# Optimization experiments

Measured on AMD Instinct MI355X. Metric: run time of the kernel, lower is better.

The kernel has to match this reference:

```python
import jax, jax.numpy as jnp
import numpy as np

N, E, D, H, G, C = 50000, 600000, 128, 128, 512, 1000
HP = H // 5  # attention-MLP bottleneck (hidden_dim // 5)


def setup_inputs() -> dict:
    key = jax.random.key(0)
    ks = jax.random.split(key, 18)
    cfg_nodes = jax.random.normal(ks[0], (N, D), jnp.float32)
    cfg_relations = jax.random.randint(ks[1], (2, E), 0, N, dtype=jnp.int32)
    pos = jnp.sort(jax.random.randint(ks[2], (G + 1,), 0, N, dtype=jnp.int32))
    node_pos = pos.at[0].set(0).at[-1].set(N)

    def lin(k, fi, fo):
        return jax.random.normal(k, (fi, fo), jnp.float32) / np.sqrt(fi)

    return dict(
        cfg_nodes=cfg_nodes, cfg_relations=cfg_relations, node_pos=node_pos,
        # GATConv layer 1 (in=D, out=H, heads=1)
        W_g1=lin(ks[3], D, H),
        att_src1=jax.random.normal(ks[4], (H,), jnp.float32) / np.sqrt(H),
        att_dst1=jax.random.normal(ks[5], (H,), jnp.float32) / np.sqrt(H),
        b_g1=jnp.zeros((H,), jnp.float32),
        # GATConv layer 2 (in=H, out=H, heads=1, concat=False)
        W_g2=lin(ks[6], H, H),
        att_src2=jax.random.normal(ks[7], (H,), jnp.float32) / np.sqrt(H),
        att_dst2=jax.random.normal(ks[8], (H,), jnp.float32) / np.sqrt(H),
        b_g2=jnp.zeros((H,), jnp.float32),
        # GraphLocalAttention projection MLP
        Wp1=lin(ks[9], H, HP), bp1=jnp.zeros((HP,), jnp.float32),
        Wp2=jax.random.normal(ks[10], (HP,), jnp.float32) / np.sqrt(HP),
        bp2=jnp.zeros((), jnp.float32),
        # final classifier
        Wl=lin(ks[11], H, C), bl=jnp.zeros((C,), jnp.float32),
    )


def _gat_conv(x, src, dst, W, a_src, a_dst, b, n_nodes):
    # PyG GATConv (heads=1): h = xW; e_ij = LeakyReLU(a_s.h_j + a_d.h_i);
    # alpha = softmax over incoming edges of each target; out_i = sum alpha*h_j + b
    h = x @ W                                    # [N, F]
    as_ = h @ a_src                              # [N]
    ad_ = h @ a_dst                              # [N]
    e = jax.nn.leaky_relu(as_[src] + ad_[dst], 0.2)   # [E]
    m = jax.ops.segment_max(e, dst, num_segments=n_nodes)
    ex = jnp.exp(e - m[dst])
    s = jax.ops.segment_sum(ex, dst, num_segments=n_nodes)
    alpha = ex / s[dst]
    out = jax.ops.segment_sum(alpha[:, None] * h[src], dst, num_segments=n_nodes)
    return out + b


def reference(cfg_nodes, cfg_relations, node_pos,
              W_g1, att_src1, att_dst1, b_g1,
              W_g2, att_src2, att_dst2, b_g2,
              Wp1, bp1, Wp2, bp2, Wl, bl):
    n = cfg_nodes.shape[0]
    # add self-loops (PyG GATConv default)
    loops = jnp.arange(n, dtype=cfg_relations.dtype)
    src = jnp.concatenate([cfg_relations[0], loops])
    dst = jnp.concatenate([cfg_relations[1], loops])
    # dropout layers are identity in eval mode
    x = _gat_conv(cfg_nodes, src, dst, W_g1, att_src1, att_dst1, b_g1, n)
    x = jax.nn.elu(x)
    x = _gat_conv(x, src, dst, W_g2, att_src2, att_dst2, b_g2, n)
    # ragged segment attention pooling (attn_by_batch, fully vectorized)
    energy = jax.nn.relu(x @ Wp1 + bp1) @ Wp2 + bp2          # [N]
    seg = jnp.clip(jnp.searchsorted(node_pos, jnp.arange(n), side='right') - 1, 0, G - 1)
    m = jax.ops.segment_max(energy, seg, num_segments=G)
    ex = jnp.exp(energy - m[seg])
    s = jax.ops.segment_sum(ex, seg, num_segments=G)
    w = ex / s[seg]                                           # per-segment softmax
    pooled = jax.ops.segment_sum(w[:, None] * x, seg, num_segments=G)  # [G, H]
    return pooled @ Wl + bl                                   # [G, C]
```

## Files before the change

### kernel.cpp

```cpp
#include <hip/hip_runtime.h>
#include <hip/hip_bf16.h>
#include <math.h>

#define WAVE 64
#define GR 32

typedef __attribute__((ext_vector_type(8))) _Float16 half8;
typedef __attribute__((ext_vector_type(4))) float f32x4;
typedef __attribute__((ext_vector_type(4))) _Float16 half4;

__global__ void count_pack(const int* __restrict__ dst, int* __restrict__ deg, int E, int nbC,
                           const float* __restrict__ W1, const float* __restrict__ W2,
                           _Float16* __restrict__ W1h, _Float16* __restrict__ W2h,
                           const float* __restrict__ Wp1, int HP,
                           _Float16* __restrict__ Ph) {
    int b = blockIdx.x;
    if (b < nbC) {
        int e = (b * 256 + threadIdx.x) * 2;
        if (e + 1 < E) {
            int2 d = *(const int2*)(dst + e);
            atomicAdd(&deg[d.x], 1);
            atomicAdd(&deg[d.y], 1);
        } else if (e < E) {
            atomicAdd(&deg[dst[e]], 1);
        }
    } else if (b < nbC + 128) {
        int pb = b - nbC;
        const float* W = (pb >= 64) ? W2 : W1;
        _Float16* Hf = (pb >= 64) ? W2h : W1h;
        int idx = (pb & 63) * 256 + threadIdx.x;
        int j = idx & 7;
        int lane = (idx >> 3) & 63;
        int kc = (idx >> 9) & 3;
        int nt = idx >> 11;
        int k = kc * 32 + (lane >> 4) * 8 + j;
        int ncol = nt * 16 + (lane & 15);
        Hf[idx] = (_Float16)W[k * 128 + ncol];
    } else {
        int idx = (b - nbC - 128) * 256 + threadIdx.x;
        int j = idx & 7;
        int lane = (idx >> 3) & 63;
        int kc = (idx >> 9) & 3;
        int nt = idx >> 11;
        int k = kc * 32 + (lane >> 4) * 8 + j;
        int ncol = nt * 16 + (lane & 15);
        float x = (ncol < HP) ? Wp1[k * HP + ncol] : 0.f;
        Ph[idx] = (_Float16)x;
    }
}

__global__ void pack_wl(const float* __restrict__ Wl, int C, _Float16* __restrict__ Wlh) {
    int idx = blockIdx.x * 256 + threadIdx.x;
    int j = idx & 7;
    int lane = (idx >> 3) & 63;
    int kc = (idx >> 9) & 3;
    int nt = idx >> 11;
    int k = kc * 32 + (lane >> 4) * 8 + j;
    int ncol = nt * 16 + (lane & 15);
    float x = (ncol < C) ? Wl[(size_t)k * C + ncol] : 0.f;
    Wlh[idx] = (_Float16)x;
}

__global__ void scan_block(const int* __restrict__ in, int* __restrict__ part,
                           int* __restrict__ bsums, int n) {
    __shared__ int tmp[256];
    int tid = threadIdx.x;
    int i = blockIdx.x * 256 + tid;
    int v = (i < n) ? in[i] : 0;
    tmp[tid] = v;
    __syncthreads();
    for (int o = 1; o < 256; o <<= 1) {
        int t = (tid >= o) ? tmp[tid - o] : 0;
        __syncthreads();
        tmp[tid] += t;
        __syncthreads();
    }
    if (i < n) part[i] = tmp[tid] - v;
    if (tid == 255) bsums[blockIdx.x] = tmp[255];
}

__global__ void scan_finish(const int* __restrict__ part, const int* __restrict__ bsums,
                            int* __restrict__ offs, int* __restrict__ cursor,
                            int n, int Etot) {
    __shared__ int acc[256];
    int b = blockIdx.x, tid = threadIdx.x;
    int s = 0;
    for (int i = tid; i < b; i += 256) s += bsums[i];
    acc[tid] = s;
    __syncthreads();
    for (int o = 128; o > 0; o >>= 1) {
        if (tid < o) acc[tid] += acc[tid + o];
        __syncthreads();
    }
    int prefix = acc[0];
    int i = b * 256 + tid;
    if (i < n) {
        int v = part[i] + prefix;
        offs[i] = v;
        cursor[i] = v;
    }
    if (b == 0 && tid == 0) offs[n] = Etot;
}

__global__ void scatter_edges(const int* __restrict__ src, const int* __restrict__ dst,
                              int* __restrict__ cursor, int* __restrict__ csr_src, int E) {
    int e0 = (blockIdx.x * 256 + threadIdx.x) * 8;
    if (e0 + 7 < E) {
        int4 d0 = *(const int4*)(dst + e0);
        int4 d1 = *(const int4*)(dst + e0 + 4);
        int4 s0 = *(const int4*)(src + e0);
        int4 s1 = *(const int4*)(src + e0 + 4);
        int p0 = atomicAdd(&cursor[d0.x], 1);
        int p1 = atomicAdd(&cursor[d0.y], 1);
        int p2 = atomicAdd(&cursor[d0.z], 1);
        int p3 = atomicAdd(&cursor[d0.w], 1);
        int p4 = atomicAdd(&cursor[d1.x], 1);
        int p5 = atomicAdd(&cursor[d1.y], 1);
        int p6 = atomicAdd(&cursor[d1.z], 1);
        int p7 = atomicAdd(&cursor[d1.w], 1);
        csr_src[p0] = s0.x;
        csr_src[p1] = s0.y;
        csr_src[p2] = s0.z;
        csr_src[p3] = s0.w;
        csr_src[p4] = s1.x;
        csr_src[p5] = s1.y;
        csr_src[p6] = s1.z;
        csr_src[p7] = s1.w;
    } else {
        for (int e = e0; e < E; ++e) {
            int p = atomicAdd(&cursor[dst[e]], 1);
            csr_src[p] = src[e];
        }
    }
}

__global__ __launch_bounds__(256) void gemm_mfma(const float* __restrict__ X,
                                                 const _Float16* __restrict__ Bh,
                                                 const float* __restrict__ a_s,
                                                 const float* __restrict__ a_d,
                                                 _Float16* __restrict__ Hout,
                                                 float* __restrict__ as_,
                                                 float* __restrict__ ad_, int n) {
    __shared__ char lds[GR * 136 * 4];
    _Float16* Xh = (_Float16*)lds;
    float* Hs = (float*)lds;

    int tid = threadIdx.x;
    int base = blockIdx.x * GR;
    const float4* X4 = (const float4*)X;

#pragma unroll
    for (int i = 0; i < 4; ++i) {
        int idx = i * 256 + tid;
        int row = idx >> 5, c4 = idx & 31;
        int rs = base + row; if (rs >= n) rs = n - 1;
        float4 v = X4[(size_t)rs * 32 + c4];
        half4 hv = {(_Float16)v.x, (_Float16)v.y, (_Float16)v.z, (_Float16)v.w};
        *(half4*)(Xh + row * 136 + c4 * 4) = hv;
    }
    __syncthreads();

    int wid = tid >> 6, lane = tid & 63;
    int quad = lane >> 4, l16 = lane & 15;
    int rowA = (wid & 1) * 16 + l16;
    int ntb = (wid >> 1) * 4;

    f32x4 acc[4];
#pragma unroll
    for (int t = 0; t < 4; ++t) acc[t] = (f32x4){0.f, 0.f, 0.f, 0.f};

    for (int kc = 0; kc < 4; ++kc) {
        half8 Ah = *(const half8*)(Xh + rowA * 136 + kc * 32 + quad * 8);
#pragma unroll
        for (int nt = 0; nt < 4; ++nt) {
            half8 Bv = *(const half8*)(Bh + (((size_t)((ntb + nt) * 4 + kc)) * 64 + lane) * 8);
            acc[nt] = __builtin_amdgcn_mfma_f32_16x16x32_f16(Ah, Bv, acc[nt], 0, 0, 0);
        }
    }
    __syncthreads();

    int rowD0 = (wid & 1) * 16 + quad * 4;
#pragma unroll
    for (int nt = 0; nt < 4; ++nt)
#pragma unroll
        for (int r = 0; r < 4; ++r)
            Hs[(rowD0 + r) * 136 + (ntb + nt) * 16 + l16] = acc[nt][r];
    __syncthreads();

    const float4* Hs4 = (const float4*)Hs;
    half4* H4 = (half4*)Hout;
#pragma unroll
    for (int i = 0; i < 4; ++i) {
        int idx = i * 256 + tid;
        int row = idx >> 5, c4 = idx & 31;
        int grow = base + row;
        if (grow < n) {
            float4 v = Hs4[row * 34 + c4];
            half4 hv = {(_Float16)v.x, (_Float16)v.y, (_Float16)v.z, (_Float16)v.w};
            H4[(size_t)grow * 32 + c4] = hv;
        }
    }

    int drow = tid >> 3, q = tid & 7;
    const float4* as4 = (const float4*)a_s;
    const float4* ad4 = (const float4*)a_d;
    float s = 0.f, d = 0.f;
#pragma unroll
    for (int j = 0; j < 4; ++j) {
        float4 v = Hs4[drow * 34 + q * 4 + j];
        float4 a = as4[q * 4 + j];
        float4 b = ad4[q * 4 + j];
        s += v.x * a.x + v.y * a.y + v.z * a.z + v.w * a.w;
        d += v.x * b.x + v.y * b.y + v.z * b.z + v.w * b.w;
    }
    s += __shfl_xor(s, 1, WAVE); s += __shfl_xor(s, 2, WAVE); s += __shfl_xor(s, 4, WAVE);
    d += __shfl_xor(d, 1, WAVE); d += __shfl_xor(d, 2, WAVE); d += __shfl_xor(d, 4, WAVE);
    if (q == 0 && base + drow < n) {
        as_[base + drow] = s;
        ad_[base + drow] = d;
    }
}

__global__ __launch_bounds__(256) void gemm_mfma_h(const _Float16* __restrict__ X,
                                                   const _Float16* __restrict__ Bh,
                                                   const float* __restrict__ a_s,
                                                   const float* __restrict__ a_d,
                                                   _Float16* __restrict__ Hout,
                                                   float* __restrict__ as_,
                                                   float* __restrict__ ad_, int n) {
    __shared__ char lds[GR * 136 * 4];
    _Float16* Xh = (_Float16*)lds;
    float* Hs = (float*)lds;

    int tid = threadIdx.x;
    int base = blockIdx.x * GR;
    const half8* X8 = (const half8*)X;

#pragma unroll
    for (int i = 0; i < 2; ++i) {
        int idx = i * 256 + tid;
        int row = idx >> 4, c8 = idx & 15;
        int rs = base + row; if (rs >= n) rs = n - 1;
        *(half8*)(Xh + row * 136 + c8 * 8) = X8[(size_t)rs * 16 + c8];
    }
    __syncthreads();

    int wid = tid >> 6, lane = tid & 63;
    int quad = lane >> 4, l16 = lane & 15;
    int rowA = (wid & 1) * 16 + l16;
    int ntb = (wid >> 1) * 4;

    f32x4 acc[4];
#pragma unroll
    for (int t = 0; t < 4; ++t) acc[t] = (f32x4){0.f, 0.f, 0.f, 0.f};

    for (int kc = 0; kc < 4; ++kc) {
        half8 Ah = *(const half8*)(Xh + rowA * 136 + kc * 32 + quad * 8);
#pragma unroll
        for (int nt = 0; nt < 4; ++nt) {
            half8 Bv = *(const half8*)(Bh + (((size_t)((ntb + nt) * 4 + kc)) * 64 + lane) * 8);
            acc[nt] = __builtin_amdgcn_mfma_f32_16x16x32_f16(Ah, Bv, acc[nt], 0, 0, 0);
        }
    }
    __syncthreads();

    int rowD0 = (wid & 1) * 16 + quad * 4;
#pragma unroll
    for (int nt = 0; nt < 4; ++nt)
#pragma unroll
        for (int r = 0; r < 4; ++r)
            Hs[(rowD0 + r) * 136 + (ntb + nt) * 16 + l16] = acc[nt][r];
    __syncthreads();

    const float4* Hs4 = (const float4*)Hs;
    half4* H4 = (half4*)Hout;
#pragma unroll
    for (int i = 0; i < 4; ++i) {
        int idx = i * 256 + tid;
        int row = idx >> 5, c4 = idx & 31;
        int grow = base + row;
        if (grow < n) {
            float4 v = Hs4[row * 34 + c4];
            half4 hv = {(_Float16)v.x, (_Float16)v.y, (_Float16)v.z, (_Float16)v.w};
            H4[(size_t)grow * 32 + c4] = hv;
        }
    }

    int drow = tid >> 3, q = tid & 7;
    const float4* as4 = (const float4*)a_s;
    const float4* ad4 = (const float4*)a_d;
    float s = 0.f, d = 0.f;
#pragma unroll
    for (int j = 0; j < 4; ++j) {
        float4 v = Hs4[drow * 34 + q * 4 + j];
        float4 a = as4[q * 4 + j];
        float4 b = ad4[q * 4 + j];
        s += v.x * a.x + v.y * a.y + v.z * a.z + v.w * a.w;
        d += v.x * b.x + v.y * b.y + v.z * b.z + v.w * b.w;
    }
    s += __shfl_xor(s, 1, WAVE); s += __shfl_xor(s, 2, WAVE); s += __shfl_xor(s, 4, WAVE);
    d += __shfl_xor(d, 1, WAVE); d += __shfl_xor(d, 2, WAVE); d += __shfl_xor(d, 4, WAVE);
    if (q == 0 && base + drow < n) {
        as_[base + drow] = s;
        ad_[base + drow] = d;
    }
}

__device__ __forceinline__ float leaky02(float x) { return x > 0.f ? x : 0.2f * x; }

__global__ __launch_bounds__(256) void edge_weights(const int* __restrict__ csr_src,
                                                    const float* __restrict__ as_,
                                                    int2* __restrict__ sw, int E) {
    int i = (blockIdx.x * 256 + threadIdx.x) * 4;
    if (i + 3 < E) {
        int4 s = *(const int4*)(csr_src + i);
        float ax = as_[s.x];
        float ay = as_[s.y];
        float az = as_[s.z];
        float aw = as_[s.w];
        int4 lo = make_int4(s.x, __float_as_int(ax), s.y, __float_as_int(ay));
        int4 hi = make_int4(s.z, __float_as_int(az), s.w, __float_as_int(aw));
        *(int4*)(sw + i) = lo;
        *(int4*)(sw + i + 2) = hi;
    } else {
        for (; i < E; ++i) {
            int s = csr_src[i];
            sw[i] = make_int2(s, __float_as_int(as_[s]));
        }
    }
}

__global__ __launch_bounds__(256) void gat_aggregate(const _Float16* __restrict__ h,
                                                     const int2* __restrict__ sw,
                                                     const float* __restrict__ as_,
                                                     const float* __restrict__ ad_,
                                                     const int* __restrict__ offs,
                                                     const float* __restrict__ bias,
                                                     _Float16* __restrict__ out, int n, int act) {
    int node = blockIdx.x * 4 + (threadIdx.x >> 6);
    int lane = threadIdx.x & 63;
    if (node >= n) return;
    int beg = offs[node], end = offs[node + 1];
    int q4 = lane >> 4, l = lane & 15;
    const half8* h8 = (const half8*)h;

    float adn = ad_[node];
    float w_self = __expf(leaky02(as_[node] + adn));
    float facc[8], facc2[8];
    {
        half8 v = h8[(size_t)node * 16 + l];
        float ws = (q4 == 0) ? w_self : 0.f;
#pragma unroll
        for (int i = 0; i < 8; ++i) { facc[i] = ws * (float)v[i]; facc2[i] = 0.f; }
    }
    float sacc = (lane == 0) ? w_self : 0.f;
    for (int j = beg; j < end; j += 8) {
        int j0 = j + q4;
        int j1 = j + 4 + q4;
        bool vA = j0 < end;
        bool vB = j1 < end;
        int jA = vA ? j0 : (end - 1);
        int jB = vB ? j1 : (end - 1);
        int2 eA = sw[jA];
        int2 eB = sw[jB];
        int sA = vA ? eA.x : node;
        int sB = vB ? eB.x : node;
        half8 a = h8[(size_t)sA * 16 + l];
        half8 b = h8[(size_t)sB * 16 + l];
        float wA = vA ? __expf(leaky02(__int_as_float(eA.y) + adn)) : 0.f;
        float wB = vB ? __expf(leaky02(__int_as_float(eB.y) + adn)) : 0.f;
#pragma unroll
        for (int i = 0; i < 8; ++i) {
            facc[i]  = fmaf(wA, (float)a[i], facc[i]);
            facc2[i] = fmaf(wB, (float)b[i], facc2[i]);
        }
        sacc += (l == 0) ? (wA + wB) : 0.f;
    }
#pragma unroll
    for (int i = 0; i < 8; ++i) {
        facc[i] += facc2[i];
        facc[i] += __shfl_xor(facc[i], 16, WAVE);
        facc[i] += __shfl_xor(facc[i], 32, WAVE);
    }
    sacc += __shfl_xor(sacc, 16, WAVE);
    sacc += __shfl_xor(sacc, 32, WAVE);
    float inv_s = 1.f / __shfl(sacc, 0, WAVE);
    if (q4 == 0) {
        const float4* b4 = (const float4*)bias;
        float4 b0 = b4[l * 2], b1 = b4[l * 2 + 1];
        float o[8];
        o[0] = fmaf(facc[0], inv_s, b0.x);
        o[1] = fmaf(facc[1], inv_s, b0.y);
        o[2] = fmaf(facc[2], inv_s, b0.z);
        o[3] = fmaf(facc[3], inv_s, b0.w);
        o[4] = fmaf(facc[4], inv_s, b1.x);
        o[5] = fmaf(facc[5], inv_s, b1.y);
        o[6] = fmaf(facc[6], inv_s, b1.z);
        o[7] = fmaf(facc[7], inv_s, b1.w);
        if (act == 1) {
#pragma unroll
            for (int i = 0; i < 8; ++i) o[i] = o[i] > 0.f ? o[i] : expm1f(o[i]);
        }
        half8 hv;
#pragma unroll
        for (int i = 0; i < 8; ++i) hv[i] = (_Float16)o[i];
        ((half8*)(out + (size_t)node * 128))[l] = hv;
    }
}

#define GR2 64
__global__ __launch_bounds__(256) void energy_mfma(const _Float16* __restrict__ X,
                                                   const _Float16* __restrict__ Ph,
                                                   const float* __restrict__ bp1,
                                                   const float* __restrict__ Wp2,
                                                   const float* __restrict__ bp2,
                                                   float* __restrict__ energy, int n, int HP) {
    __shared__ _Float16 Xh[GR2 * 136];
    int tid = threadIdx.x;
    int base = blockIdx.x * GR2;
    const half8* X8 = (const half8*)X;
#pragma unroll
    for (int i = 0; i < 4; ++i) {
        int idx = i * 256 + tid;
        int row = idx >> 4, c8 = idx & 15;
        int rs = base + row; if (rs >= n) rs = n - 1;
        *(half8*)(Xh + row * 136 + c8 * 8) = X8[(size_t)rs * 16 + c8];
    }
    __syncthreads();

    int wid = tid >> 6, lane = tid & 63;
    int quad = lane >> 4, l16 = lane & 15;
    int rowA = wid * 16 + l16;

    f32x4 acc0 = (f32x4){0.f, 0.f, 0.f, 0.f};
    f32x4 acc1 = (f32x4){0.f, 0.f, 0.f, 0.f};
    for (int kc = 0; kc < 4; ++kc) {
        half8 Ah = *(const half8*)(Xh + rowA * 136 + kc * 32 + quad * 8);
        half8 B0 = *(const half8*)(Ph + (((size_t)kc) * 64 + lane) * 8);
        half8 B1 = *(const half8*)(Ph + (((size_t)(4 + kc)) * 64 + lane) * 8);
        acc0 = __builtin_amdgcn_mfma_f32_16x16x32_f16(Ah, B0, acc0, 0, 0, 0);
        acc1 = __builtin_amdgcn_mfma_f32_16x16x32_f16(Ah, B1, acc1, 0, 0, 0);
    }

    float b0 = bp1[l16];
    float w0 = Wp2[l16];
    int c1 = 16 + l16;
    int c1c = c1 < HP ? c1 : HP - 1;
    float b1 = bp1[c1c];
    float w1 = (c1 < HP) ? Wp2[c1c] : 0.f;
    float bp2v = bp2[0];
#pragma unroll
    for (int r = 0; r < 4; ++r) {
        float h0 = acc0[r] + b0;
        h0 = h0 > 0.f ? h0 : 0.f;
        float h1 = acc1[r] + b1;
        h1 = h1 > 0.f ? h1 : 0.f;
        float v = h0 * w0 + h1 * w1;
        v += __shfl_xor(v, 1, WAVE);
        v += __shfl_xor(v, 2, WAVE);
        v += __shfl_xor(v, 4, WAVE);
        v += __shfl_xor(v, 8, WAVE);
        int row = base + wid * 16 + quad * 4 + r;
        if (l16 == 0 && row < n) energy[row] = v + bp2v;
    }
}

__global__ __launch_bounds__(256) void seg_pool(const _Float16* __restrict__ X,
                                                const float* __restrict__ energy,
                                                const int* __restrict__ node_pos,
                                                float* __restrict__ pooled) {
    int g = blockIdx.x >> 1;
    int bn = blockIdx.x & 1;
    int beg = node_pos[g], end = node_pos[g + 1];
    int tid = threadIdx.x;
    int wid = tid >> 6, lane = tid & 63;
    __shared__ float swr[8];
    __shared__ float4 red[256];

    float m = -INFINITY;
    for (int i = beg + tid; i < end; i += 256) m = fmaxf(m, energy[i]);
#pragma unroll
    for (int o = 1; o < 64; o <<= 1) m = fmaxf(m, __shfl_xor(m, o, WAVE));
    if (lane == 0) swr[wid] = m;
    __syncthreads();
    m = fmaxf(fmaxf(swr[0], swr[1]), fmaxf(swr[2], swr[3]));

    float s = 0.f;
    for (int i = beg + tid; i < end; i += 256) s += __expf(energy[i] - m);
#pragma unroll
    for (int o = 1; o < 64; o <<= 1) s += __shfl_xor(s, o, WAVE);
    if (lane == 0) swr[4 + wid] = s;
    __syncthreads();
    s = swr[4] + swr[5] + swr[6] + swr[7];
    float inv = (end > beg && s > 0.f) ? 1.f / s : 0.f;

    int cq = tid & 15;
    int rg = tid >> 4;
    const half4* X4 = (const half4*)X;
    float4 acc = make_float4(0.f, 0.f, 0.f, 0.f);
#pragma unroll 2
    for (int i = beg + rg; i < end; i += 16) {
        float w = __expf(energy[i] - m) * inv;
        half4 v = X4[(size_t)i * 32 + bn * 16 + cq];
        acc.x = fmaf(w, (float)v.x, acc.x);
        acc.y = fmaf(w, (float)v.y, acc.y);
        acc.z = fmaf(w, (float)v.z, acc.z);
        acc.w = fmaf(w, (float)v.w, acc.w);
    }
    red[tid] = acc;
#pragma unroll
    for (int o = 8; o >= 1; o >>= 1) {
        __syncthreads();
        if (rg < o) {
            float4 t = red[tid + o * 16];
            acc.x += t.x; acc.y += t.y; acc.z += t.z; acc.w += t.w;
            red[tid] = acc;
        }
    }
    if (rg == 0)
        ((float4*)(pooled + (size_t)g * 128 + bn * 64))[cq] = acc;
}

__global__ __launch_bounds__(256) void classify_mfma(const float* __restrict__ P,
                                                     const _Float16* __restrict__ Wlh,
                                                     const float* __restrict__ bl,
                                                     float* __restrict__ out,
                                                     int G_, int C, int nbM) {
    __shared__ _Float16 Xh[GR * 136];
    int tid = threadIdx.x;
    int bm = blockIdx.x % nbM;
    int bn = blockIdx.x / nbM;
    int base = bm * GR;
    const float4* X4 = (const float4*)P;
#pragma unroll
    for (int i = 0; i < 4; ++i) {
        int idx = i * 256 + tid;
        int row = idx >> 5, c4 = idx & 31;
        int rs = base + row; if (rs >= G_) rs = G_ - 1;
        float4 v = X4[(size_t)rs * 32 + c4];
        half4 hv = {(_Float16)v.x, (_Float16)v.y, (_Float16)v.z, (_Float16)v.w};
        *(half4*)(Xh + row * 136 + c4 * 4) = hv;
    }
    __syncthreads();

    int wid = tid >> 6, lane = tid & 63;
    int quad = lane >> 4, l16 = lane & 15;
    int rowA = (wid & 1) * 16 + l16;
    int ntb = bn * 8 + (wid >> 1) * 4;

    f32x4 acc[4];
#pragma unroll
    for (int t = 0; t < 4; ++t) acc[t] = (f32x4){0.f, 0.f, 0.f, 0.f};

    for (int kc = 0; kc < 4; ++kc) {
        half8 Ah = *(const half8*)(Xh + rowA * 136 + kc * 32 + quad * 8);
#pragma unroll
        for (int nt = 0; nt < 4; ++nt) {
            half8 Bv = *(const half8*)(Wlh + (((size_t)((ntb + nt) * 4 + kc)) * 64 + lane) * 8);
            acc[nt] = __builtin_amdgcn_mfma_f32_16x16x32_f16(Ah, Bv, acc[nt], 0, 0, 0);
        }
    }

    int row0 = base + (wid & 1) * 16 + quad * 4;
#pragma unroll
    for (int nt = 0; nt < 4; ++nt) {
        int col = (ntb + nt) * 16 + l16;
        if (col < C) {
            float b = bl[col];
#pragma unroll
            for (int r = 0; r < 4; ++r) {
                int row = row0 + r;
                if (row < G_) out[(size_t)row * C + col] = acc[nt][r] + b;
            }
        }
    }
}

extern "C" void kernel_launch(void* const* d_in, const int* in_sizes, int n_in,
                              void* d_out, int out_size, void* d_ws, size_t ws_size,
                              hipStream_t stream) {
    const float* cfg_nodes = (const float*)d_in[0];
    const int* rel = (const int*)d_in[1];
    const int* node_pos = (const int*)d_in[2];
    const float* W_g1 = (const float*)d_in[3];
    const float* att_src1 = (const float*)d_in[4];
    const float* att_dst1 = (const float*)d_in[5];
    const float* b_g1 = (const float*)d_in[6];
    const float* W_g2 = (const float*)d_in[7];
    const float* att_src2 = (const float*)d_in[8];
    const float* att_dst2 = (const float*)d_in[9];
    const float* b_g2 = (const float*)d_in[10];
    const float* Wp1 = (const float*)d_in[11];
    const float* bp1 = (const float*)d_in[12];
    const float* Wp2 = (const float*)d_in[13];
    const float* bp2 = (const float*)d_in[14];
    const float* Wl = (const float*)d_in[15];
    const float* bl = (const float*)d_in[16];

    const int N = in_sizes[0] / 128;
    const int E = in_sizes[1] / 2;
    const int G = in_sizes[2] - 1;
    const int HP = in_sizes[12];
    const int C = out_size / G;

    const int* srcArr = rel;
    const int* dstArr = rel + E;

    char* w = (char*)d_ws;
    auto carve = [&](size_t bytes) -> char* {
        char* p = w;
        w += (bytes + 255) & ~(size_t)255;
        return p;
    };
    _Float16* bufH = (_Float16*)carve((size_t)N * 128 * 2);
    _Float16* bufF = (_Float16*)carve((size_t)N * 128 * 2);
    float* asv = (float*)carve((size_t)N * 4);
    float* adv = (float*)carve((size_t)N * 4);
    float* energy = (float*)carve((size_t)N * 4);
    int* deg = (int*)carve((size_t)N * 4);
    int* offs = (int*)carve((size_t)(N + 1) * 4);
    int* cursor = (int*)carve((size_t)N * 4);
    int* csr_src = (int*)carve((size_t)E * 4);
    int2* swbuf = (int2*)carve((size_t)E * 8);
    int* bsums = (int*)carve(1024);
    _Float16* W1h = (_Float16*)carve(16384 * 2);
    _Float16* W2h = (_Float16*)carve(16384 * 2);
    _Float16* Ph = (_Float16*)carve(4096 * 2);
    _Float16* Wlh = (_Float16*)carve(131072 * 2);
    float* pooled = (float*)carve((size_t)G * 128 * 4);

    const int nbN = (N + 255) / 256;
    const int nbC = ((E + 1) / 2 + 255) / 256;
    const int nbS = ((E + 7) / 8 + 255) / 256;
    const int nbT = (N + GR - 1) / GR;
    const int nbT2 = (N + GR2 - 1) / GR2;
    const int nbW = (E + 1023) / 1024;
    const int nbM = (G + GR - 1) / GR;
    const int nbCt = (C + 127) / 128;

    hipMemsetAsync(deg, 0, (size_t)N * 4, stream);
    count_pack<<<nbC + 144, 256, 0, stream>>>(dstArr, deg, E, nbC,
                                              W_g1, W_g2, W1h, W2h, Wp1, HP, Ph);
    pack_wl<<<512, 256, 0, stream>>>(Wl, C, Wlh);
    scan_block<<<nbN, 256, 0, stream>>>(deg, offs, bsums, N);
    scan_finish<<<nbN, 256, 0, stream>>>(offs, bsums, offs, cursor, N, E);
    scatter_edges<<<nbS, 256, 0, stream>>>(srcArr, dstArr, cursor, csr_src, E);

    gemm_mfma<<<nbT, 256, 0, stream>>>(cfg_nodes, W1h, att_src1, att_dst1,
                                       bufH, asv, adv, N);
    edge_weights<<<nbW, 256, 0, stream>>>(csr_src, asv, swbuf, E);
    gat_aggregate<<<(N + 3) / 4, 256, 0, stream>>>(bufH, swbuf, asv, adv, offs, b_g1, bufF, N, 1);

    gemm_mfma_h<<<nbT, 256, 0, stream>>>(bufF, W2h, att_src2, att_dst2,
                                         bufH, asv, adv, N);
    edge_weights<<<nbW, 256, 0, stream>>>(csr_src, asv, swbuf, E);
    gat_aggregate<<<(N + 3) / 4, 256, 0, stream>>>(bufH, swbuf, asv, adv, offs, b_g2, bufF, N, 0);

    energy_mfma<<<nbT2, 256, 0, stream>>>(bufF, Ph, bp1, Wp2, bp2, energy, N, HP);
    seg_pool<<<G * 2, 256, 0, stream>>>(bufF, energy, node_pos, pooled);
    classify_mfma<<<nbM * nbCt, 256, 0, stream>>>(pooled, Wlh, bl, (float*)d_out, G, C, nbM);
}
```

Measured before the change: 295.0 us.

## Fuse edge-weight gather into aggregation and fold Wl packing into count_pack

Removes the edge_weights kernel, which built an interleaved (src, as_[src]) buffer per layer; gat_aggregate now reads csr_src and gathers as_[src] directly. The pack_wl kernel is folded into count_pack as extra blocks. This cuts two launches and an E*8-byte write+read per layer, at the cost of a dependent random gather of as_ inside the aggregation loop. Invalid lanes now clamp to end-1 rather than substituting the node index, which is harmless because their weight is zero.

```diff
diff --git a/kernel.cpp b/kernel.cpp
--- a/kernel.cpp
+++ b/kernel.cpp
@@ -13,7 +13,9 @@
                            const float* __restrict__ W1, const float* __restrict__ W2,
                            _Float16* __restrict__ W1h, _Float16* __restrict__ W2h,
                            const float* __restrict__ Wp1, int HP,
-                           _Float16* __restrict__ Ph) {
+                           _Float16* __restrict__ Ph,
+                           const float* __restrict__ Wl, int C,
+                           _Float16* __restrict__ Wlh) {
     int b = blockIdx.x;
     if (b < nbC) {
         int e = (b * 256 + threadIdx.x) * 2;
@@ -36,7 +38,7 @@
         int k = kc * 32 + (lane >> 4) * 8 + j;
         int ncol = nt * 16 + (lane & 15);
         Hf[idx] = (_Float16)W[k * 128 + ncol];
-    } else {
+    } else if (b < nbC + 144) {
         int idx = (b - nbC - 128) * 256 + threadIdx.x;
         int j = idx & 7;
         int lane = (idx >> 3) & 63;
@@ -46,19 +48,17 @@
         int ncol = nt * 16 + (lane & 15);
         float x = (ncol < HP) ? Wp1[k * HP + ncol] : 0.f;
         Ph[idx] = (_Float16)x;
-    }
-}
-
-__global__ void pack_wl(const float* __restrict__ Wl, int C, _Float16* __restrict__ Wlh) {
-    int idx = blockIdx.x * 256 + threadIdx.x;
-    int j = idx & 7;
-    int lane = (idx >> 3) & 63;
-    int kc = (idx >> 9) & 3;
-    int nt = idx >> 11;
-    int k = kc * 32 + (lane >> 4) * 8 + j;
-    int ncol = nt * 16 + (lane & 15);
-    float x = (ncol < C) ? Wl[(size_t)k * C + ncol] : 0.f;
-    Wlh[idx] = (_Float16)x;
+    } else {
+        int idx = (b - nbC - 144) * 256 + threadIdx.x;
+        int j = idx & 7;
+        int lane = (idx >> 3) & 63;
+        int kc = (idx >> 9) & 3;
+        int nt = idx >> 11;
+        int k = kc * 32 + (lane >> 4) * 8 + j;
+        int ncol = nt * 16 + (lane & 15);
+        float x = (ncol < C) ? Wl[(size_t)k * C + ncol] : 0.f;
+        Wlh[idx] = (_Float16)x;
+    }
 }
 
 __global__ void scan_block(const int* __restrict__ in, int* __restrict__ part,
@@ -308,30 +308,8 @@
 
 __device__ __forceinline__ float leaky02(float x) { return x > 0.f ? x : 0.2f * x; }
 
-__global__ __launch_bounds__(256) void edge_weights(const int* __restrict__ csr_src,
-                                                    const float* __restrict__ as_,
-                                                    int2* __restrict__ sw, int E) {
-    int i = (blockIdx.x * 256 + threadIdx.x) * 4;
-    if (i + 3 < E) {
-        int4 s = *(const int4*)(csr_src + i);
-        float ax = as_[s.x];
-        float ay = as_[s.y];
-        float az = as_[s.z];
-        float aw = as_[s.w];
-        int4 lo = make_int4(s.x, __float_as_int(ax), s.y, __float_as_int(ay));
-        int4 hi = make_int4(s.z, __float_as_int(az), s.w, __float_as_int(aw));
-        *(int4*)(sw + i) = lo;
-        *(int4*)(sw + i + 2) = hi;
-    } else {
-        for (; i < E; ++i) {
-            int s = csr_src[i];
-            sw[i] = make_int2(s, __float_as_int(as_[s]));
-        }
-    }
-}
-
 __global__ __launch_bounds__(256) void gat_aggregate(const _Float16* __restrict__ h,
-                                                     const int2* __restrict__ sw,
+                                                     const int* __restrict__ csr_src,
                                                      const float* __restrict__ as_,
                                                      const float* __restrict__ ad_,
                                                      const int* __restrict__ offs,
@@ -356,19 +334,19 @@
     float sacc = (lane == 0) ? w_self : 0.f;
     for (int j = beg; j < end; j += 8) {
         int j0 = j + q4;
-        int j1 = j + 4 + q4;
+        int j1 = j0 + 4;
         bool vA = j0 < end;
         bool vB = j1 < end;
         int jA = vA ? j0 : (end - 1);
         int jB = vB ? j1 : (end - 1);
-        int2 eA = sw[jA];
-        int2 eB = sw[jB];
-        int sA = vA ? eA.x : node;
-        int sB = vB ? eB.x : node;
+        int sA = csr_src[jA];
+        int sB = csr_src[jB];
         half8 a = h8[(size_t)sA * 16 + l];
         half8 b = h8[(size_t)sB * 16 + l];
-        float wA = vA ? __expf(leaky02(__int_as_float(eA.y) + adn)) : 0.f;
-        float wB = vB ? __expf(leaky02(__int_as_float(eB.y) + adn)) : 0.f;
+        float asA = as_[sA];
+        float asB = as_[sB];
+        float wA = vA ? __expf(leaky02(asA + adn)) : 0.f;
+        float wB = vB ? __expf(leaky02(asB + adn)) : 0.f;
 #pragma unroll
         for (int i = 0; i < 8; ++i) {
             facc[i]  = fmaf(wA, (float)a[i], facc[i]);
@@ -621,7 +599,6 @@
     int* offs = (int*)carve((size_t)(N + 1) * 4);
     int* cursor = (int*)carve((size_t)N * 4);
     int* csr_src = (int*)carve((size_t)E * 4);
-    int2* swbuf = (int2*)carve((size_t)E * 8);
     int* bsums = (int*)carve(1024);
     _Float16* W1h = (_Float16*)carve(16384 * 2);
     _Float16* W2h = (_Float16*)carve(16384 * 2);
@@ -634,27 +611,24 @@
     const int nbS = ((E + 7) / 8 + 255) / 256;
     const int nbT = (N + GR - 1) / GR;
     const int nbT2 = (N + GR2 - 1) / GR2;
-    const int nbW = (E + 1023) / 1024;
     const int nbM = (G + GR - 1) / GR;
     const int nbCt = (C + 127) / 128;
 
     hipMemsetAsync(deg, 0, (size_t)N * 4, stream);
-    count_pack<<<nbC + 144, 256, 0, stream>>>(dstArr, deg, E, nbC,
-                                              W_g1, W_g2, W1h, W2h, Wp1, HP, Ph);
-    pack_wl<<<512, 256, 0, stream>>>(Wl, C, Wlh);
+    count_pack<<<nbC + 656, 256, 0, stream>>>(dstArr, deg, E, nbC,
+                                              W_g1, W_g2, W1h, W2h, Wp1, HP, Ph,
+                                              Wl, C, Wlh);
     scan_block<<<nbN, 256, 0, stream>>>(deg, offs, bsums, N);
     scan_finish<<<nbN, 256, 0, stream>>>(offs, bsums, offs, cursor, N, E);
     scatter_edges<<<nbS, 256, 0, stream>>>(srcArr, dstArr, cursor, csr_src, E);
 
     gemm_mfma<<<nbT, 256, 0, stream>>>(cfg_nodes, W1h, att_src1, att_dst1,
                                        bufH, asv, adv, N);
-    edge_weights<<<nbW, 256, 0, stream>>>(csr_src, asv, swbuf, E);
-    gat_aggregate<<<(N + 3) / 4, 256, 0, stream>>>(bufH, swbuf, asv, adv, offs, b_g1, bufF, N, 1);
+    gat_aggregate<<<(N + 3) / 4, 256, 0, stream>>>(bufH, csr_src, asv, adv, offs, b_g1, bufF, N, 1);
 
     gemm_mfma_h<<<nbT, 256, 0, stream>>>(bufF, W2h, att_src2, att_dst2,
                                          bufH, asv, adv, N);
-    edge_weights<<<nbW, 256, 0, stream>>>(csr_src, asv, swbuf, E);
-    gat_aggregate<<<(N + 3) / 4, 256, 0, stream>>>(bufH, swbuf, asv, adv, offs, b_g2, bufF, N, 0);
+    gat_aggregate<<<(N + 3) / 4, 256, 0, stream>>>(bufH, csr_src, asv, adv, offs, b_g2, bufF, N, 0);
 
     energy_mfma<<<nbT2, 256, 0, stream>>>(bufF, Ph, bp1, Wp2, bp2, energy, N, HP);
     seg_pool<<<G * 2, 256, 0, stream>>>(bufF, energy, node_pos, pooled);
```

After: 285.0 us. 1.04x faster.
